# Optimization experiments

Measured on AMD Instinct MI355X. Metric: run time of the kernel, lower is better.

## Reference

```python
import jax, jax.numpy as jnp
import numpy as np


def setup_inputs() -> dict:
    key = jax.random.key(0)
    k1, k2 = jax.random.split(key)
    n, d, ic, oc, r = 128, 256, 16, 16, 10
    x = jax.random.normal(k1, (n, d, ic, r), dtype=jnp.float32)
    weights = jax.random.normal(k2, (d, ic, oc, r), dtype=jnp.float32)
    return {"x": x, "weights": weights}


def reference(x, weights):
    # x: [n, d, ic, r]; weights: [d, ic, oc, r]
    # log_softmax over in_channels (dim=1 of weights)
    log_weights = jax.nn.log_softmax(weights, axis=1)  # [d, ic, oc, r]
    # broadcast add: x[n,d,ic,1,r] + lw[d,ic,oc,r] -> [n,d,ic,oc,r]
    z = x[:, :, :, None, :] + log_weights[None]
    # logsumexp over ic -> [n, d, oc, r]
    return jax.nn.logsumexp(z, axis=2)
```

## Files before the change

kernel.cpp:

```cpp
#include <hip/hip_runtime.h>
#include <hip/hip_bf16.h>


#define EROW 20
#define WROW 20
#define RSP  164

__device__ __forceinline__ void stage_x_chunk(__hip_bfloat16* exs, const float4& a,
                                              const float4& b, int seg8, int colw) {
    float vals[8] = {a.x, a.y, a.z, a.w, b.x, b.y, b.z, b.w};
#pragma unroll
    for (int k = 0; k < 8; ++k)
        exs[(seg8 * 8 + k) * EROW + colw] = __float2bfloat16(__expf(vals[k]));
}

__device__ __forceinline__ void compute_chunk(const __hip_bfloat16* exs,
                                              const __hip_bfloat16* wes,
                                              int r, int ng, int oc4, float acc[2][4]) {
#pragma unroll
    for (int i = 0; i < 2; ++i)
#pragma unroll
        for (int j = 0; j < 4; ++j) acc[i][j] = 0.f;
#pragma unroll
    for (int ic = 0; ic < 16; ++ic) {
        const int icr = ic * 10 + r;
        const int cb = (((ng >> 1) ^ ((icr >> 3) & 3)) << 2) + ((ng & 1) << 1);
        const unsigned eu = *reinterpret_cast<const unsigned*>(&exs[icr * EROW + cb]);
        const uint2 wu = *reinterpret_cast<const uint2*>(&wes[icr * WROW + (oc4 << 2)]);
        const float e0 = __uint_as_float(eu << 16);
        const float e1 = __uint_as_float(eu & 0xFFFF0000u);
        const float w0 = __uint_as_float(wu.x << 16);
        const float w1 = __uint_as_float(wu.x & 0xFFFF0000u);
        const float w2 = __uint_as_float(wu.y << 16);
        const float w3 = __uint_as_float(wu.y & 0xFFFF0000u);
        acc[0][0] = fmaf(e0, w0, acc[0][0]);
        acc[0][1] = fmaf(e0, w1, acc[0][1]);
        acc[0][2] = fmaf(e0, w2, acc[0][2]);
        acc[0][3] = fmaf(e0, w3, acc[0][3]);
        acc[1][0] = fmaf(e1, w0, acc[1][0]);
        acc[1][1] = fmaf(e1, w1, acc[1][1]);
        acc[1][2] = fmaf(e1, w2, acc[1][2]);
        acc[1][3] = fmaf(e1, w3, acc[1][3]);
    }
}

__device__ __forceinline__ void epilogue_chunk(float* res, const float* lcs,
                                               int r, int ng, int oc4, float acc[2][4]) {
#pragma unroll
    for (int j = 0; j < 4; ++j) {
        const int ocr = ((oc4 << 2) + j) * 10 + r;
        const float lcj = lcs[ocr];
#pragma unroll
        for (int i = 0; i < 2; ++i) {
            const int n = (ng << 1) + i;
            const int q = (ocr >> 2) ^ (n & 7);
            res[n * RSP + (q << 2) + (ocr & 3)] = __logf(acc[i][j]) - lcj;
        }
    }
}

__device__ __forceinline__ void store_chunk(const float* res, float* __restrict__ out,
                                            int nbase, int d, int n_l, int seg8) {
    const int f = n_l & 7;
    const float4 v0 = *reinterpret_cast<const float4*>(&res[n_l * RSP + ((((seg8 << 1) | 0) ^ f) << 2)]);
    const float4 v1 = *reinterpret_cast<const float4*>(&res[n_l * RSP + ((((seg8 << 1) | 1) ^ f) << 2)]);
    float* og = out + ((nbase + n_l) * 256 + d) * 160 + seg8 * 8;
    *reinterpret_cast<float4*>(og)     = v0;
    *reinterpret_cast<float4*>(og + 4) = v1;
}

__global__ __launch_bounds__(320, 5) void fused_lse_kernel(const float* __restrict__ x,
                                                           const float* __restrict__ w,
                                                           float* __restrict__ out) {
    __shared__ __align__(16) __hip_bfloat16 exs[160 * EROW];
    __shared__ __align__(16) __hip_bfloat16 wes[160 * WROW];
    __shared__ float lcs[160];
    __shared__ __align__(16) float res[16 * RSP];

    const int tid     = threadIdx.x;
    const int d       = blockIdx.x & 255;
    const int n_super = (blockIdx.x >> 8) << 5;

    const int n_l  = tid / 20;
    const int seg8 = tid % 20;
    const int colw = (((n_l >> 2) ^ (seg8 & 3)) << 2) + (n_l & 3);

    const float* xg0 = x + ((n_super + n_l) * 256 + d) * 160 + seg8 * 8;
    const float* xg1 = x + ((n_super + 16 + n_l) * 256 + d) * 160 + seg8 * 8;
    const float4* wg = reinterpret_cast<const float4*>(w + d * 2560);

    const float4 xa0 = *reinterpret_cast<const float4*>(xg0);
    const float4 xb0 = *reinterpret_cast<const float4*>(xg0 + 4);
    const float4 wa  = wg[tid * 2];
    const float4 wb  = wg[tid * 2 + 1];
    const float4 xa1 = *reinterpret_cast<const float4*>(xg1);
    const float4 xb1 = *reinterpret_cast<const float4*>(xg1 + 4);

    {
        float vals[8] = {wa.x, wa.y, wa.z, wa.w, wb.x, wb.y, wb.z, wb.w};
        const int base = tid * 8;
#pragma unroll
        for (int k = 0; k < 8; ++k) {
            const int off = base + k;
            const int ic  = off / 160;
            const int ocr = off - ic * 160;
            const int oc  = ocr / 10;
            const int r   = ocr - oc * 10;
            wes[(ic * 10 + r) * WROW + oc] = __float2bfloat16(__expf(vals[k]));
        }
    }
    stage_x_chunk(exs, xa0, xb0, seg8, colw);
    __syncthreads();

    if (tid < 160) {
        const int oc = tid / 10, rr = tid - (tid / 10) * 10;
        float s = 0.f;
#pragma unroll
        for (int ic = 0; ic < 16; ++ic)
            s += __bfloat162float(wes[(ic * 10 + rr) * WROW + oc]);
        lcs[tid] = __logf(s);
    }

    const int r   = tid >> 5;
    const int ng  = (tid >> 2) & 7;
    const int oc4 = tid & 3;

    float acc[2][4];
    compute_chunk(exs, wes, r, ng, oc4, acc);
    __syncthreads();

    stage_x_chunk(exs, xa1, xb1, seg8, colw);
    epilogue_chunk(res, lcs, r, ng, oc4, acc);
    __syncthreads();

    store_chunk(res, out, n_super, d, n_l, seg8);
    compute_chunk(exs, wes, r, ng, oc4, acc);
    __syncthreads();

    epilogue_chunk(res, lcs, r, ng, oc4, acc);
    __syncthreads();

    store_chunk(res, out, n_super + 16, d, n_l, seg8);
}

extern "C" void kernel_launch(void* const* d_in, const int* in_sizes, int n_in,
                              void* d_out, int out_size, void* d_ws, size_t ws_size,
                              hipStream_t stream) {
    const float* x = (const float*)d_in[0];
    const float* w = (const float*)d_in[1];
    float* out = (float*)d_out;

    fused_lse_kernel<<<1024, 320, 0, stream>>>(x, w, out);
}
```

Baseline: 18.23 us.

## Process four n-chunks per block with double-buffered shared staging

Each block now covers 64 batch rows instead of 32, so the grid shrinks to 512 blocks. The exp/log-sum of the weights is amortised over more rows. The x staging and result buffers are double-buffered so loads, staging, compute and stores of successive chunks overlap. The costs are higher shared memory per block, a lower occupancy hint (launch bounds 5 to 2), fewer blocks to fill the 256 CUs, and more registers held by prefetched x values.

New measurement: 19.06 us. +4.6%, slower.

```diff
diff --git a/kernel.cpp b/kernel.cpp
--- a/kernel.cpp
+++ b/kernel.cpp
@@ -6,7 +6,9 @@
 #define WROW 20
 #define RSP  164
 
-__device__ __forceinline__ void stage_x_chunk(__hip_bfloat16* exs, const float4& a,
+using bf16 = __hip_bfloat16;
+
+__device__ __forceinline__ void stage_x_chunk(bf16* exs, const float4& a,
                                               const float4& b, int seg8, int colw) {
     float vals[8] = {a.x, a.y, a.z, a.w, b.x, b.y, b.z, b.w};
 #pragma unroll
@@ -14,8 +16,7 @@
         exs[(seg8 * 8 + k) * EROW + colw] = __float2bfloat16(__expf(vals[k]));
 }
 
-__device__ __forceinline__ void compute_chunk(const __hip_bfloat16* exs,
-                                              const __hip_bfloat16* wes,
+__device__ __forceinline__ void compute_chunk(const bf16* exs, const bf16* wes,
                                               int r, int ng, int oc4, float acc[2][4]) {
 #pragma unroll
     for (int i = 0; i < 2; ++i)
@@ -69,33 +70,34 @@
     *reinterpret_cast<float4*>(og + 4) = v1;
 }
 
-__global__ __launch_bounds__(320, 5) void fused_lse_kernel(const float* __restrict__ x,
+__global__ __launch_bounds__(320, 2) void fused_lse_kernel(const float* __restrict__ x,
                                                            const float* __restrict__ w,
                                                            float* __restrict__ out) {
-    __shared__ __align__(16) __hip_bfloat16 exs[160 * EROW];
-    __shared__ __align__(16) __hip_bfloat16 wes[160 * WROW];
+    __shared__ __align__(16) bf16 wes[160 * WROW];
+    __shared__ __align__(16) bf16 exsA[160 * EROW];
+    __shared__ __align__(16) bf16 exsB[160 * EROW];
     __shared__ float lcs[160];
-    __shared__ __align__(16) float res[16 * RSP];
+    __shared__ __align__(16) float resA[16 * RSP];
+    __shared__ __align__(16) float resB[16 * RSP];
 
-    const int tid     = threadIdx.x;
-    const int d       = blockIdx.x & 255;
-    const int n_super = (blockIdx.x >> 8) << 5;
+    const int tid = threadIdx.x;
+    const int d   = blockIdx.x & 255;
+    const int nb  = (blockIdx.x >> 8) << 6;
 
     const int n_l  = tid / 20;
     const int seg8 = tid % 20;
     const int colw = (((n_l >> 2) ^ (seg8 & 3)) << 2) + (n_l & 3);
 
-    const float* xg0 = x + ((n_super + n_l) * 256 + d) * 160 + seg8 * 8;
-    const float* xg1 = x + ((n_super + 16 + n_l) * 256 + d) * 160 + seg8 * 8;
+    const float* xbase = x + ((nb + n_l) * 256 + d) * 160 + seg8 * 8;
+    const int CS = 16 * 256 * 160;
+
     const float4* wg = reinterpret_cast<const float4*>(w + d * 2560);
-
-    const float4 xa0 = *reinterpret_cast<const float4*>(xg0);
-    const float4 xb0 = *reinterpret_cast<const float4*>(xg0 + 4);
-    const float4 wa  = wg[tid * 2];
-    const float4 wb  = wg[tid * 2 + 1];
-    const float4 xa1 = *reinterpret_cast<const float4*>(xg1);
-    const float4 xb1 = *reinterpret_cast<const float4*>(xg1 + 4);
-
+    const float4 wa = wg[tid * 2];
+    const float4 wb = wg[tid * 2 + 1];
+    const float4 a0 = *reinterpret_cast<const float4*>(xbase);
+    const float4 b0 = *reinterpret_cast<const float4*>(xbase + 4);
+    const float4 a1 = *reinterpret_cast<const float4*>(xbase + CS);
+    const float4 b1 = *reinterpret_cast<const float4*>(xbase + CS + 4);
     {
         float vals[8] = {wa.x, wa.y, wa.z, wa.w, wb.x, wb.y, wb.z, wb.w};
         const int base = tid * 8;
@@ -109,9 +111,11 @@
             wes[(ic * 10 + r) * WROW + oc] = __float2bfloat16(__expf(vals[k]));
         }
     }
-    stage_x_chunk(exs, xa0, xb0, seg8, colw);
+    stage_x_chunk(exsA, a0, b0, seg8, colw);
     __syncthreads();
 
+    const float4 a2 = *reinterpret_cast<const float4*>(xbase + 2 * CS);
+    const float4 b2 = *reinterpret_cast<const float4*>(xbase + 2 * CS + 4);
     if (tid < 160) {
         const int oc = tid / 10, rr = tid - (tid / 10) * 10;
         float s = 0.f;
@@ -120,27 +124,43 @@
             s += __bfloat162float(wes[(ic * 10 + rr) * WROW + oc]);
         lcs[tid] = __logf(s);
     }
-
     const int r   = tid >> 5;
     const int ng  = (tid >> 2) & 7;
     const int oc4 = tid & 3;
-
-    float acc[2][4];
-    compute_chunk(exs, wes, r, ng, oc4, acc);
+    float accX[2][4], accY[2][4];
+    compute_chunk(exsA, wes, r, ng, oc4, accX);
+    stage_x_chunk(exsB, a1, b1, seg8, colw);
     __syncthreads();
 
-    stage_x_chunk(exs, xa1, xb1, seg8, colw);
-    epilogue_chunk(res, lcs, r, ng, oc4, acc);
+    const float4 a3 = *reinterpret_cast<const float4*>(xbase + 3 * CS);
+    const float4 b3 = *reinterpret_cast<const float4*>(xbase + 3 * CS + 4);
+    stage_x_chunk(exsA, a2, b2, seg8, colw);
+    epilogue_chunk(resA, lcs, r, ng, oc4, accX);
     __syncthreads();
 
-    store_chunk(res, out, n_super, d, n_l, seg8);
-    compute_chunk(exs, wes, r, ng, oc4, acc);
+    store_chunk(resA, out, nb + 0, d, n_l, seg8);
+    compute_chunk(exsB, wes, r, ng, oc4, accY);
     __syncthreads();
 
-    epilogue_chunk(res, lcs, r, ng, oc4, acc);
+    stage_x_chunk(exsB, a3, b3, seg8, colw);
+    epilogue_chunk(resB, lcs, r, ng, oc4, accY);
     __syncthreads();
 
-    store_chunk(res, out, n_super + 16, d, n_l, seg8);
+    store_chunk(resB, out, nb + 16, d, n_l, seg8);
+    compute_chunk(exsA, wes, r, ng, oc4, accX);
+    __syncthreads();
+
+    epilogue_chunk(resA, lcs, r, ng, oc4, accX);
+    __syncthreads();
+
+    store_chunk(resA, out, nb + 32, d, n_l, seg8);
+    compute_chunk(exsB, wes, r, ng, oc4, accY);
+    __syncthreads();
+
+    epilogue_chunk(resB, lcs, r, ng, oc4, accY);
+    __syncthreads();
+
+    store_chunk(resB, out, nb + 48, d, n_l, seg8);
 }
 
 extern "C" void kernel_launch(void* const* d_in, const int* in_sizes, int n_in,
@@ -150,5 +170,5 @@
     const float* w = (const float*)d_in[1];
     float* out = (float*)d_out;
 
-    fused_lse_kernel<<<1024, 320, 0, stream>>>(x, w, out);
+    fused_lse_kernel<<<512, 320, 0, stream>>>(x, w, out);
 }
```
